# Kernel tuning notes

Measured on AMD Instinct MI355X. Metric: run time of the kernel, lower is better.

The kernel has to match this reference:

```python
import jax, jax.numpy as jnp
import numpy as np

N = 100000
E = 1600000
IN_DIM = 128
OUT_DIM = 64


def setup_inputs() -> dict:
    key = jax.random.key(0)
    k_h, k_ei, k_ew, k_W, k_a = jax.random.split(key, 5)
    h = jax.random.normal(k_h, (N, IN_DIM), dtype=jnp.float32)
    edge_index = jax.random.randint(k_ei, (2, E), 0, N, dtype=jnp.int64)
    edge_weight = jax.random.uniform(k_ew, (E,), dtype=jnp.float32)
    # nn.Linear weights (Kaiming-uniform-ish scale)
    W = jax.random.uniform(k_W, (OUT_DIM, IN_DIM), dtype=jnp.float32,
                           minval=-1.0, maxval=1.0) / np.sqrt(IN_DIM)
    a = jax.random.uniform(k_a, (2 * OUT_DIM,), dtype=jnp.float32,
                           minval=-1.0, maxval=1.0) / np.sqrt(2 * OUT_DIM)
    return {"h": h, "edge_index": edge_index, "edge_weight": edge_weight,
            "W": W, "a": a}


def reference(h, edge_index, edge_weight, W, a):
    # Faithful translation of _GATConvSparse.forward (inference; dropout = identity).
    n = h.shape[0]
    src, dst = edge_index[0], edge_index[1]
    Wh = h @ W.T                                  # (N, out_dim)
    d = Wh.shape[1]
    # a(cat([Wh[src], Wh[dst]])) == Wh[src] @ a[:d] + Wh[dst] @ a[d:]
    alpha = Wh[src] @ a[:d] + Wh[dst] @ a[d:]     # (E,)
    alpha = alpha * edge_weight
    # Buggy-but-faithful 'softmax': segment-sum raw scores onto dst nodes...
    alpha_node = jax.ops.segment_sum(alpha, dst, num_segments=n)   # (N,)
    alpha_exp = jnp.exp(alpha_node - alpha_node.max())             # (N,)
    # ...then normalize per-edge exp(src) by sum of exp(src) over each dst segment.
    denom = jax.ops.segment_sum(alpha_exp[src], dst, num_segments=n)  # (N,)
    alpha_norm = alpha_exp[src] / (denom[dst] + 1e-9)              # (E,)
    out = jax.ops.segment_sum(alpha_norm[:, None] * Wh[src], dst,
                              num_segments=n)                      # (N, out_dim)
    return jax.nn.elu(out)
```

## Files before the change

### kernel.cpp

```cpp
#include <hip/hip_runtime.h>
#include <math.h>

#define Nn 100000
#define Ee 1600000
#define IND 128
#define OUTD 64
#define DPB 64
#define NB 1563
#define BSTR 1280
#define CAP 1536
#define GB 1563
#define EB_BLOCKS 391
#define CSCAN_BLOCKS 196
#define AFIX 1048576.0f

using bf16x8 = __attribute__((ext_vector_type(8))) short;
using f32x4 = __attribute__((ext_vector_type(4))) float;

__device__ __forceinline__ unsigned short f2bf(float f) {
    unsigned u = __float_as_uint(f);
    u = u + 0x7FFFu + ((u >> 16) & 1u);
    return (unsigned short)(u >> 16);
}
__device__ __forceinline__ float bf2f(unsigned short h) {
    return __uint_as_float(((unsigned)h) << 16);
}

__device__ __forceinline__ bool probe64(const void* __restrict__ ei) {
    const long long* p = (const long long*)ei;
    bool ok = true;
#pragma unroll
    for (int i = 0; i < 8; ++i) {
        long long v = p[i];
        ok = ok && (v >= 0 && v < Nn);
    }
    return ok;
}

__device__ __forceinline__ void load_edge(const void* ei, int e, bool is64,
                                          int& s, int& d) {
    if (is64) {
        const long long* p = (const long long*)ei;
        s = (int)p[e];
        d = (int)p[Ee + e];
    } else {
        const int* p = (const int*)ei;
        s = p[e];
        d = p[Ee + e];
    }
}

__device__ __forceinline__ int load_dst(const void* ei, int e, bool is64) {
    if (is64) return (int)((const long long*)ei)[Ee + e];
    return ((const int*)ei)[Ee + e];
}

__global__ __launch_bounds__(256) void k_fused(
    const float* __restrict__ h, const float* __restrict__ W,
    const float* __restrict__ a, unsigned short* __restrict__ Whb,
    float* __restrict__ s1, float* __restrict__ s2,
    const void* __restrict__ ei, unsigned short* __restrict__ counts) {
    __shared__ unsigned short Ash[64][136];
    __shared__ unsigned short Wsh[64][136];
    __shared__ float al[2 * OUTD];
    int bid = blockIdx.x;
    int t = threadIdx.x;

    if (bid < GB) {
        int R = bid * 64;
        for (int i = t; i < 2048; i += 256) {
            float4 v = ((const float4*)W)[i];
            int r = i >> 5, c = (i & 31) << 2;
            unsigned lo = (unsigned)f2bf(v.x) | ((unsigned)f2bf(v.y) << 16);
            unsigned hi = (unsigned)f2bf(v.z) | ((unsigned)f2bf(v.w) << 16);
            *(uint2*)&Wsh[r][c] = make_uint2(lo, hi);
        }
        if (t < 32) ((float4*)al)[t] = ((const float4*)a)[t];
        for (int i = t; i < 2048; i += 256) {
            int r = i >> 5, c = (i & 31) << 2;
            int n = R + r;
            float4 v = make_float4(0.f, 0.f, 0.f, 0.f);
            if (n < Nn) v = ((const float4*)(h + (size_t)n * IND))[i & 31];
            unsigned lo = (unsigned)f2bf(v.x) | ((unsigned)f2bf(v.y) << 16);
            unsigned hi = (unsigned)f2bf(v.z) | ((unsigned)f2bf(v.w) << 16);
            *(uint2*)&Ash[r][c] = make_uint2(lo, hi);
        }
        __syncthreads();

        int w = t >> 6, l = t & 63;
        int li = l & 15, lg = l >> 4;
        f32x4 acc[4];
#pragma unroll
        for (int nt = 0; nt < 4; ++nt) acc[nt] = (f32x4){0.f, 0.f, 0.f, 0.f};
#pragma unroll
        for (int kk = 0; kk < 4; ++kk) {
            bf16x8 af = *(const bf16x8*)&Ash[w * 16 + li][kk * 32 + lg * 8];
#pragma unroll
            for (int nt = 0; nt < 4; ++nt) {
                bf16x8 bf = *(const bf16x8*)&Wsh[nt * 16 + li][kk * 32 + lg * 8];
                acc[nt] = __builtin_amdgcn_mfma_f32_16x16x32_bf16(af, bf,
                                                                  acc[nt],
                                                                  0, 0, 0);
            }
        }
        float p1[4] = {0.f, 0.f, 0.f, 0.f};
        float p2[4] = {0.f, 0.f, 0.f, 0.f};
#pragma unroll
        for (int nt = 0; nt < 4; ++nt) {
            float a1v = al[nt * 16 + li];
            float a2v = al[OUTD + nt * 16 + li];
#pragma unroll
            for (int r = 0; r < 4; ++r) {
                float v = acc[nt][r];
                p1[r] += v * a1v;
                p2[r] += v * a2v;
                int row = R + w * 16 + lg * 4 + r;
                if (row < Nn)
                    Whb[(size_t)row * OUTD + nt * 16 + li] = f2bf(v);
            }
        }
#pragma unroll
        for (int r = 0; r < 4; ++r) {
#pragma unroll
            for (int m = 1; m < 16; m <<= 1) {
                p1[r] += __shfl_xor(p1[r], m, 64);
                p2[r] += __shfl_xor(p2[r], m, 64);
            }
        }
        if (li < 4) {
            int row = R + w * 16 + lg * 4 + li;
            if (row < Nn) {
                s1[row] = p1[li];
                s2[row] = p2[li];
            }
        }
    } else {
        int* cnt = (int*)&Ash[0][0];
        for (int i = t; i < NB; i += 256) cnt[i] = 0;
        __syncthreads();
        bool is64 = probe64(ei);
        int hc = bid - GB;
        int base = hc * 4096;
#pragma unroll
        for (int i = 0; i < 16; ++i) {
            int e = base + i * 256 + t;
            if (e < Ee) atomicAdd(&cnt[load_dst(ei, e, is64) >> 6], 1);
        }
        __syncthreads();
        for (int i = t; i < NB; i += 256)
            counts[(size_t)hc * NB + i] = (unsigned short)cnt[i];
    }
}

__global__ __launch_bounds__(512) void k_cscan(
    unsigned short* __restrict__ counts, int* __restrict__ bcnt) {
    int gw = (int)((blockIdx.x * 512 + threadIdx.x) >> 6);
    int lane = threadIdx.x & 63;
    if (gw >= NB) return;
    int run = 0;
    for (int c0 = 0; c0 < EB_BLOCKS; c0 += 64) {
        int c = c0 + lane;
        int v = (c < EB_BLOCKS) ? (int)counts[(size_t)c * NB + gw] : 0;
        int s = v;
#pragma unroll
        for (int d = 1; d < 64; d <<= 1) {
            int u = __shfl_up(s, d, 64);
            if (lane >= d) s += u;
        }
        if (c < EB_BLOCKS)
            counts[(size_t)c * NB + gw] = (unsigned short)(run + s - v);
        run += __shfl(s, 63, 64);
    }
    if (lane == 0) bcnt[gw] = run;
}

__global__ __launch_bounds__(512) void k_binscatter(
    const void* __restrict__ ei, const float* __restrict__ ew,
    const float* __restrict__ s1, const float* __restrict__ s2,
    const unsigned short* __restrict__ counts, uint2* __restrict__ bins) {
    __shared__ int cnt[NB];
    __shared__ int gbase[NB];
    int hc = blockIdx.x;
    for (int i = threadIdx.x; i < NB; i += 512) {
        cnt[i] = 0;
        gbase[i] = (int)counts[(size_t)hc * NB + i];
    }
    __syncthreads();
    bool is64 = probe64(ei);
    int base = hc * 4096;
    unsigned rx[8];
    int ryi[8];
    int rb[8];
    int rk[8];
#pragma unroll
    for (int i = 0; i < 8; ++i) {
        int e = base + i * 512 + threadIdx.x;
        rb[i] = -1;
        rx[i] = 0;
        ryi[i] = 0;
        rk[i] = 0;
        if (e < Ee) {
            int s, d;
            load_edge(ei, e, is64, s, d);
            float alpha = (s1[s] + s2[d]) * ew[e];
            ryi[i] = (int)rintf(alpha * AFIX);
            int b = d >> 6;
            rb[i] = b;
            rk[i] = atomicAdd(&cnt[b], 1);
            rx[i] = ((unsigned)s << 7) | ((unsigned)(d & 63) << 24);
        }
    }
    __syncthreads();
#pragma unroll
    for (int i = 0; i < 8; ++i) {
        if (rb[i] >= 0) {
            int off = gbase[rb[i]] + rk[i];
            if (off < BSTR)
                bins[(size_t)rb[i] * BSTR + off] =
                    make_uint2(rx[i], (unsigned)ryi[i]);
        }
    }
}

__global__ __launch_bounds__(256) void k_balpha(
    const uint2* __restrict__ bins, const int* __restrict__ bcnt,
    float* __restrict__ ae) {
    __shared__ int anl[DPB];
    int b = blockIdx.x;
    int t = threadIdx.x;
    if (t < DPB) anl[t] = 0;
    __syncthreads();
    int e0 = b * BSTR;
    int c = bcnt[b];
    int e1 = e0 + (c < BSTR ? c : BSTR);
    for (int k = e0 + t; k < e1; k += 256) {
        uint2 r = bins[k];
        atomicAdd(&anl[r.x >> 24], (int)r.y);
    }
    __syncthreads();
    if (t < DPB) {
        int n = b * DPB + t;
        if (n < Nn) ae[n] = expf((float)anl[t] * (1.f / AFIX));
    }
}

#define AGG_BODY(NR)                                                         \
    {                                                                        \
        uint2 rr[NR];                                                        \
        unsigned ww[NR];                                                     \
        _Pragma("unroll") for (int j = 0; j < NR; ++j)                       \
            rr[j] = lp[2 * j];                                               \
        _Pragma("unroll") for (int j = 0; j < NR; ++j)                       \
            ww[j] = *(const unsigned*)(whbB + (rr[j].x + hl4));              \
        _Pragma("unroll") for (int j = 0; j < NR; ++j) {                     \
            float aa = __uint_as_float(rr[j].y);                             \
            acc.x += aa * __uint_as_float(ww[j] << 16);                      \
            acc.y += aa * __uint_as_float(ww[j] & 0xFFFF0000u);              \
            den += aa;                                                       \
        }                                                                    \
        lp += 2 * NR;                                                        \
    }

__global__ __launch_bounds__(512, 4) void k_agg(
    const uint2* __restrict__ bins, const int* __restrict__ bcnt,
    const float* __restrict__ ae, const unsigned short* __restrict__ Whb,
    float* __restrict__ out) {
    __shared__ uint2 lrec[CAP];
    __shared__ int cnt[DPB];
    __shared__ int sbase[DPB];
    int b = blockIdx.x;
    int t = threadIdx.x;
    int lane = t & 63;
    int wave = t >> 6;
    int half = lane >> 5;
    int hl = lane & 31;
    unsigned hl4 = (unsigned)hl << 2;
    int e0 = b * BSTR;
    int c = bcnt[b];
    int total = c < BSTR ? c : BSTR;
    int e1 = e0 + total;
    const char* whbB = (const char*)Whb;

    if (t < DPB) cnt[t] = 0;
    __syncthreads();

    unsigned su[CAP / 512];
    float sa[CAP / 512];
    int srk[CAP / 512];
#pragma unroll
    for (int i = 0; i < CAP / 512; ++i) {
        int k = e0 + i * 512 + t;
        srk[i] = -1;
        if (k < e1) {
            uint2 r = bins[k];
            srk[i] = atomicAdd(&cnt[r.x >> 24], 1);
            su[i] = r.x;
            sa[i] = ae[(r.x >> 7) & 0x1FFFF];
        }
    }
    __syncthreads();
    if (t < DPB) {
        int v = cnt[t];
#pragma unroll
        for (int d = 1; d < DPB; d <<= 1) {
            int u = __shfl_up(v, d, 64);
            if (t >= d) v += u;
        }
        sbase[t] = v;
    }
    __syncthreads();
#pragma unroll
    for (int i = 0; i < CAP / 512; ++i) {
        if (srk[i] >= 0) {
            int dloc = su[i] >> 24;
            int pos = sbase[dloc] - cnt[dloc] + srk[i];
            lrec[pos] = make_uint2(su[i] & 0x00FFFF80u,
                                   __float_as_uint(sa[i]));
        }
    }
    __syncthreads();

    for (int d = wave * 8; d < wave * 8 + 8; ++d) {
        int k1 = sbase[d];
        int k = k1 - cnt[d];
        const uint2* lp = lrec + k + half;
        float2 acc = make_float2(0.f, 0.f);
        float den = 0.f;
        for (; k + 15 < k1; k += 16) AGG_BODY(8);
        for (; k + 7 < k1; k += 8) AGG_BODY(4);
        for (; k + 1 < k1; k += 2) AGG_BODY(1);
        if (k < k1) {
            uint2 rA = lrec[k];
            unsigned wA = *(const unsigned*)(whbB + (rA.x + hl4));
            float aA = half ? 0.f : __uint_as_float(rA.y);
            acc.x += aA * __uint_as_float(wA << 16);
            acc.y += aA * __uint_as_float(wA & 0xFFFF0000u);
            den += aA;
        }
        float ax = acc.x + __shfl_xor(acc.x, 32, 64);
        float ay = acc.y + __shfl_xor(acc.y, 32, 64);
        float dn = den + __shfl_xor(den, 32, 64);
        if (half == 0) {
            int n = b * DPB + d;
            if (n < Nn) {
                float inv = 1.f / (dn + 1e-9f);
                float vx = ax * inv;
                float vy = ay * inv;
                vx = vx > 0.f ? vx : expm1f(vx);
                vy = vy > 0.f ? vy : expm1f(vy);
                *(float2*)&out[(size_t)n * OUTD + hl * 2] =
                    make_float2(vx, vy);
            }
        }
    }
}

extern "C" void kernel_launch(void* const* d_in, const int* in_sizes, int n_in,
                              void* d_out, int out_size, void* d_ws,
                              size_t ws_size, hipStream_t stream) {
    const float* h = (const float*)d_in[0];
    const void* ei = d_in[1];
    const float* ew = (const float*)d_in[2];
    const float* W = (const float*)d_in[3];
    const float* a = (const float*)d_in[4];
    float* out = (float*)d_out;

    unsigned short* Whb = (unsigned short*)d_ws;
    float* s1 = (float*)(Whb + (size_t)Nn * OUTD);
    float* s2 = s1 + Nn;
    float* ae = s2 + Nn;
    int* bcnt = (int*)(ae + Nn);
    uint2* bins = (uint2*)(bcnt + 2048);
    unsigned short* counts =
        (unsigned short*)(bins + (size_t)NB * BSTR);

    k_fused<<<GB + EB_BLOCKS, 256, 0, stream>>>(h, W, a, Whb, s1, s2, ei,
                                                counts);
    k_cscan<<<CSCAN_BLOCKS, 512, 0, stream>>>(counts, bcnt);
    k_binscatter<<<EB_BLOCKS, 512, 0, stream>>>(ei, ew, s1, s2, counts, bins);
    k_balpha<<<NB, 256, 0, stream>>>(bins, bcnt, ae);
    k_agg<<<NB, 512, 0, stream>>>(bins, bcnt, ae, Whb, out);
}
```

Before: 110.2 us.

## Overlap GEMM with edge bin-scatter by deferring alpha to per-bin pass

The histogram now runs alone, and the bin-scatter runs in the same launch as the bf16 MFMA projection. Bins store the raw edge weight instead of a precomputed alpha, so the scatter no longer has to wait for s1/s2. k_balpha rebuilds the per-node score by summing s1[src]*w and w separately, then adds s2[dst] times the weight sum. This lets the GEMM and the scatter share the GPU. In exchange, balpha does an extra random s1 gather and a second atomic per edge, and the fixed-point rounding changes slightly.

```diff
diff --git a/kernel.cpp b/kernel.cpp
--- a/kernel.cpp
+++ b/kernel.cpp
@@ -55,101 +55,23 @@
     return ((const int*)ei)[Ee + e];
 }
 
-__global__ __launch_bounds__(256) void k_fused(
-    const float* __restrict__ h, const float* __restrict__ W,
-    const float* __restrict__ a, unsigned short* __restrict__ Whb,
-    float* __restrict__ s1, float* __restrict__ s2,
+__global__ __launch_bounds__(256) void k_hist(
     const void* __restrict__ ei, unsigned short* __restrict__ counts) {
-    __shared__ unsigned short Ash[64][136];
-    __shared__ unsigned short Wsh[64][136];
-    __shared__ float al[2 * OUTD];
-    int bid = blockIdx.x;
+    __shared__ int cnt[NB];
     int t = threadIdx.x;
-
-    if (bid < GB) {
-        int R = bid * 64;
-        for (int i = t; i < 2048; i += 256) {
-            float4 v = ((const float4*)W)[i];
-            int r = i >> 5, c = (i & 31) << 2;
-            unsigned lo = (unsigned)f2bf(v.x) | ((unsigned)f2bf(v.y) << 16);
-            unsigned hi = (unsigned)f2bf(v.z) | ((unsigned)f2bf(v.w) << 16);
-            *(uint2*)&Wsh[r][c] = make_uint2(lo, hi);
-        }
-        if (t < 32) ((float4*)al)[t] = ((const float4*)a)[t];
-        for (int i = t; i < 2048; i += 256) {
-            int r = i >> 5, c = (i & 31) << 2;
-            int n = R + r;
-            float4 v = make_float4(0.f, 0.f, 0.f, 0.f);
-            if (n < Nn) v = ((const float4*)(h + (size_t)n * IND))[i & 31];
-            unsigned lo = (unsigned)f2bf(v.x) | ((unsigned)f2bf(v.y) << 16);
-            unsigned hi = (unsigned)f2bf(v.z) | ((unsigned)f2bf(v.w) << 16);
-            *(uint2*)&Ash[r][c] = make_uint2(lo, hi);
-        }
-        __syncthreads();
-
-        int w = t >> 6, l = t & 63;
-        int li = l & 15, lg = l >> 4;
-        f32x4 acc[4];
-#pragma unroll
-        for (int nt = 0; nt < 4; ++nt) acc[nt] = (f32x4){0.f, 0.f, 0.f, 0.f};
-#pragma unroll
-        for (int kk = 0; kk < 4; ++kk) {
-            bf16x8 af = *(const bf16x8*)&Ash[w * 16 + li][kk * 32 + lg * 8];
-#pragma unroll
-            for (int nt = 0; nt < 4; ++nt) {
-                bf16x8 bf = *(const bf16x8*)&Wsh[nt * 16 + li][kk * 32 + lg * 8];
-                acc[nt] = __builtin_amdgcn_mfma_f32_16x16x32_bf16(af, bf,
-                                                                  acc[nt],
-                                                                  0, 0, 0);
-            }
-        }
-        float p1[4] = {0.f, 0.f, 0.f, 0.f};
-        float p2[4] = {0.f, 0.f, 0.f, 0.f};
-#pragma unroll
-        for (int nt = 0; nt < 4; ++nt) {
-            float a1v = al[nt * 16 + li];
-            float a2v = al[OUTD + nt * 16 + li];
-#pragma unroll
-            for (int r = 0; r < 4; ++r) {
-                float v = acc[nt][r];
-                p1[r] += v * a1v;
-                p2[r] += v * a2v;
-                int row = R + w * 16 + lg * 4 + r;
-                if (row < Nn)
-                    Whb[(size_t)row * OUTD + nt * 16 + li] = f2bf(v);
-            }
-        }
-#pragma unroll
-        for (int r = 0; r < 4; ++r) {
-#pragma unroll
-            for (int m = 1; m < 16; m <<= 1) {
-                p1[r] += __shfl_xor(p1[r], m, 64);
-                p2[r] += __shfl_xor(p2[r], m, 64);
-            }
-        }
-        if (li < 4) {
-            int row = R + w * 16 + lg * 4 + li;
-            if (row < Nn) {
-                s1[row] = p1[li];
-                s2[row] = p2[li];
-            }
-        }
-    } else {
-        int* cnt = (int*)&Ash[0][0];
-        for (int i = t; i < NB; i += 256) cnt[i] = 0;
-        __syncthreads();
-        bool is64 = probe64(ei);
-        int hc = bid - GB;
-        int base = hc * 4096;
-#pragma unroll
-        for (int i = 0; i < 16; ++i) {
-            int e = base + i * 256 + t;
-            if (e < Ee) atomicAdd(&cnt[load_dst(ei, e, is64) >> 6], 1);
-        }
-        __syncthreads();
-        for (int i = t; i < NB; i += 256)
-            counts[(size_t)hc * NB + i] = (unsigned short)cnt[i];
-    }
+    int hc = blockIdx.x;
+    for (int i = t; i < NB; i += 256) cnt[i] = 0;
+    __syncthreads();
+    bool is64 = probe64(ei);
+    int base = hc * 4096;
+#pragma unroll
+    for (int i = 0; i < 16; ++i) {
+        int e = base + i * 256 + t;
+        if (e < Ee) atomicAdd(&cnt[load_dst(ei, e, is64) >> 6], 1);
+    }
+    __syncthreads();
+    for (int i = t; i < NB; i += 256)
+        counts[(size_t)hc * NB + i] = (unsigned short)cnt[i];
 }
 
 __global__ __launch_bounds__(512) void k_cscan(
@@ -174,73 +96,165 @@
     if (lane == 0) bcnt[gw] = run;
 }
 
-__global__ __launch_bounds__(512) void k_binscatter(
+__global__ __launch_bounds__(256) void k_gembin(
+    const float* __restrict__ h, const float* __restrict__ W,
+    const float* __restrict__ a, unsigned short* __restrict__ Whb,
+    float* __restrict__ s1, float* __restrict__ s2,
     const void* __restrict__ ei, const float* __restrict__ ew,
-    const float* __restrict__ s1, const float* __restrict__ s2,
     const unsigned short* __restrict__ counts, uint2* __restrict__ bins) {
-    __shared__ int cnt[NB];
-    __shared__ int gbase[NB];
-    int hc = blockIdx.x;
-    for (int i = threadIdx.x; i < NB; i += 512) {
-        cnt[i] = 0;
-        gbase[i] = (int)counts[(size_t)hc * NB + i];
-    }
-    __syncthreads();
-    bool is64 = probe64(ei);
-    int base = hc * 4096;
-    unsigned rx[8];
-    int ryi[8];
-    int rb[8];
-    int rk[8];
-#pragma unroll
-    for (int i = 0; i < 8; ++i) {
-        int e = base + i * 512 + threadIdx.x;
-        rb[i] = -1;
-        rx[i] = 0;
-        ryi[i] = 0;
-        rk[i] = 0;
-        if (e < Ee) {
-            int s, d;
-            load_edge(ei, e, is64, s, d);
-            float alpha = (s1[s] + s2[d]) * ew[e];
-            ryi[i] = (int)rintf(alpha * AFIX);
-            int b = d >> 6;
-            rb[i] = b;
-            rk[i] = atomicAdd(&cnt[b], 1);
-            rx[i] = ((unsigned)s << 7) | ((unsigned)(d & 63) << 24);
-        }
-    }
-    __syncthreads();
-#pragma unroll
-    for (int i = 0; i < 8; ++i) {
-        if (rb[i] >= 0) {
-            int off = gbase[rb[i]] + rk[i];
-            if (off < BSTR)
-                bins[(size_t)rb[i] * BSTR + off] =
-                    make_uint2(rx[i], (unsigned)ryi[i]);
+    __shared__ unsigned short Ash[64][136];
+    __shared__ unsigned short Wsh[64][136];
+    __shared__ float al[2 * OUTD];
+    int bid = blockIdx.x;
+    int t = threadIdx.x;
+
+    if (bid < EB_BLOCKS) {
+        int* cnt = (int*)&Ash[0][0];
+        int* gb = (int*)&Wsh[0][0];
+        int hc = bid;
+        for (int i = t; i < NB; i += 256) {
+            cnt[i] = 0;
+            gb[i] = (int)counts[(size_t)hc * NB + i];
+        }
+        __syncthreads();
+        bool is64 = probe64(ei);
+        int base = hc * 4096;
+#pragma unroll
+        for (int half8 = 0; half8 < 2; ++half8) {
+            unsigned rx[8];
+            unsigned rw[8];
+            int rb[8];
+            int rk[8];
+#pragma unroll
+            for (int i = 0; i < 8; ++i) {
+                int e = base + half8 * 2048 + i * 256 + t;
+                rb[i] = -1;
+                rx[i] = 0;
+                rw[i] = 0;
+                rk[i] = 0;
+                if (e < Ee) {
+                    int s, d;
+                    load_edge(ei, e, is64, s, d);
+                    rw[i] = __float_as_uint(ew[e]);
+                    int b = d >> 6;
+                    rb[i] = b;
+                    rk[i] = atomicAdd(&cnt[b], 1);
+                    rx[i] = ((unsigned)s << 7) | ((unsigned)(d & 63) << 24);
+                }
+            }
+#pragma unroll
+            for (int i = 0; i < 8; ++i) {
+                if (rb[i] >= 0) {
+                    int off = gb[rb[i]] + rk[i];
+                    if (off < BSTR)
+                        bins[(size_t)rb[i] * BSTR + off] =
+                            make_uint2(rx[i], rw[i]);
+                }
+            }
+        }
+        return;
+    }
+
+    int R = (bid - EB_BLOCKS) * 64;
+    for (int i = t; i < 2048; i += 256) {
+        float4 v = ((const float4*)W)[i];
+        int r = i >> 5, c = (i & 31) << 2;
+        unsigned lo = (unsigned)f2bf(v.x) | ((unsigned)f2bf(v.y) << 16);
+        unsigned hi = (unsigned)f2bf(v.z) | ((unsigned)f2bf(v.w) << 16);
+        *(uint2*)&Wsh[r][c] = make_uint2(lo, hi);
+    }
+    if (t < 32) ((float4*)al)[t] = ((const float4*)a)[t];
+    for (int i = t; i < 2048; i += 256) {
+        int r = i >> 5, c = (i & 31) << 2;
+        int n = R + r;
+        float4 v = make_float4(0.f, 0.f, 0.f, 0.f);
+        if (n < Nn) v = ((const float4*)(h + (size_t)n * IND))[i & 31];
+        unsigned lo = (unsigned)f2bf(v.x) | ((unsigned)f2bf(v.y) << 16);
+        unsigned hi = (unsigned)f2bf(v.z) | ((unsigned)f2bf(v.w) << 16);
+        *(uint2*)&Ash[r][c] = make_uint2(lo, hi);
+    }
+    __syncthreads();
+
+    int w = t >> 6, l = t & 63;
+    int li = l & 15, lg = l >> 4;
+    f32x4 acc[4];
+#pragma unroll
+    for (int nt = 0; nt < 4; ++nt) acc[nt] = (f32x4){0.f, 0.f, 0.f, 0.f};
+#pragma unroll
+    for (int kk = 0; kk < 4; ++kk) {
+        bf16x8 af = *(const bf16x8*)&Ash[w * 16 + li][kk * 32 + lg * 8];
+#pragma unroll
+        for (int nt = 0; nt < 4; ++nt) {
+            bf16x8 bf = *(const bf16x8*)&Wsh[nt * 16 + li][kk * 32 + lg * 8];
+            acc[nt] = __builtin_amdgcn_mfma_f32_16x16x32_bf16(af, bf,
+                                                              acc[nt],
+                                                              0, 0, 0);
+        }
+    }
+    float p1[4] = {0.f, 0.f, 0.f, 0.f};
+    float p2[4] = {0.f, 0.f, 0.f, 0.f};
+#pragma unroll
+    for (int nt = 0; nt < 4; ++nt) {
+        float a1v = al[nt * 16 + li];
+        float a2v = al[OUTD + nt * 16 + li];
+#pragma unroll
+        for (int r = 0; r < 4; ++r) {
+            float v = acc[nt][r];
+            p1[r] += v * a1v;
+            p2[r] += v * a2v;
+            int row = R + w * 16 + lg * 4 + r;
+            if (row < Nn)
+                Whb[(size_t)row * OUTD + nt * 16 + li] = f2bf(v);
+        }
+    }
+#pragma unroll
+    for (int r = 0; r < 4; ++r) {
+#pragma unroll
+        for (int m = 1; m < 16; m <<= 1) {
+            p1[r] += __shfl_xor(p1[r], m, 64);
+            p2[r] += __shfl_xor(p2[r], m, 64);
+        }
+    }
+    if (li < 4) {
+        int row = R + w * 16 + lg * 4 + li;
+        if (row < Nn) {
+            s1[row] = p1[li];
+            s2[row] = p2[li];
         }
     }
 }
 
 __global__ __launch_bounds__(256) void k_balpha(
     const uint2* __restrict__ bins, const int* __restrict__ bcnt,
+    const float* __restrict__ s1, const float* __restrict__ s2,
     float* __restrict__ ae) {
     __shared__ int anl[DPB];
+    __shared__ int ews[DPB];
     int b = blockIdx.x;
     int t = threadIdx.x;
-    if (t < DPB) anl[t] = 0;
+    if (t < DPB) {
+        anl[t] = 0;
+        ews[t] = 0;
+    }
     __syncthreads();
     int e0 = b * BSTR;
     int c = bcnt[b];
     int e1 = e0 + (c < BSTR ? c : BSTR);
     for (int k = e0 + t; k < e1; k += 256) {
         uint2 r = bins[k];
-        atomicAdd(&anl[r.x >> 24], (int)r.y);
+        int dloc = (int)(r.x >> 24);
+        int s = (int)((r.x >> 7) & 0x1FFFF);
+        float w = __uint_as_float(r.y);
+        atomicAdd(&anl[dloc], (int)rintf(s1[s] * w * AFIX));
+        atomicAdd(&ews[dloc], (int)rintf(w * AFIX));
     }
     __syncthreads();
     if (t < DPB) {
         int n = b * DPB + t;
-        if (n < Nn) ae[n] = expf((float)anl[t] * (1.f / AFIX));
+        if (n < Nn) {
+            float an = ((float)anl[t] + s2[n] * (float)ews[t]) * (1.f / AFIX);
+            ae[n] = expf(an);
+        }
     }
 }
 
@@ -374,10 +388,10 @@
     unsigned short* counts =
         (unsigned short*)(bins + (size_t)NB * BSTR);
 
-    k_fused<<<GB + EB_BLOCKS, 256, 0, stream>>>(h, W, a, Whb, s1, s2, ei,
-                                                counts);
+    k_hist<<<EB_BLOCKS, 256, 0, stream>>>(ei, counts);
     k_cscan<<<CSCAN_BLOCKS, 512, 0, stream>>>(counts, bcnt);
-    k_binscatter<<<EB_BLOCKS, 512, 0, stream>>>(ei, ew, s1, s2, counts, bins);
-    k_balpha<<<NB, 256, 0, stream>>>(bins, bcnt, ae);
+    k_gembin<<<EB_BLOCKS + GB, 256, 0, stream>>>(h, W, a, Whb, s1, s2, ei,
+                                                 ew, counts, bins);
+    k_balpha<<<NB, 256, 0, stream>>>(bins, bcnt, s1, s2, ae);
     k_agg<<<NB, 512, 0, stream>>>(bins, bcnt, ae, Whb, out);
 }
```

Result: faster. 107.1 us (-2.8%).
